# Kernel tuning notes

Measured on AMD Instinct MI355X. Metric: run time of the kernel, lower is better.

## Reference

```python
import jax, jax.numpy as jnp
import numpy as np

B, S, D, H = 2, 2048, 1024, 16
DK = D // H
NEG_INF = jnp.finfo(jnp.float32).min


def setup_inputs() -> dict:
    key = jax.random.key(0)
    ks = jax.random.split(key, 9)
    mk = lambda k, shp, s=0.02: (jax.random.normal(k, shp, dtype=jnp.float32) * s)
    return {
        "X": jax.random.normal(ks[0], (B, S, D), dtype=jnp.float32),
        "Wq": mk(ks[1], (D, D)), "bq": jnp.zeros((D,), jnp.float32),
        "Wk": mk(ks[2], (D, D)), "bk": jnp.zeros((D,), jnp.float32),
        "Wv": mk(ks[3], (D, D)), "bv": jnp.zeros((D,), jnp.float32),
        "Wo": mk(ks[4], (D, D)), "bo": jnp.zeros((D,), jnp.float32),
        "padding_mask": jnp.zeros((B, S), dtype=jnp.int32),
        "causal_mask": 1,
    }


def reference(X, Wq, bq, Wk, bk, Wv, bv, Wo, bo, padding_mask, causal_mask):
    b, s, d = X.shape
    # QKV projections (torch Linear: x @ W.T + b), split into heads -> [B,H,S,DK]
    proj = lambda W, bias: (X @ W.T + bias).reshape(b, s, H, DK).transpose(0, 2, 1, 3)
    Q, K, V = proj(Wq, bq), proj(Wk, bk), proj(Wv, bv)
    scale = jnp.sqrt(jnp.float32(DK))
    scores = jnp.einsum('bhqd,bhkd->bhqk', Q, K) / scale  # [B,H,S,S]
    if padding_mask is not None:
        scores = jnp.where(padding_mask[:, None, None, :] == 1, NEG_INF, scores)
    if causal_mask:
        causal = jnp.triu(jnp.ones((s, s), dtype=bool), k=1)  # [S,S]
        scores = jnp.where(causal[None, None, :, :], NEG_INF, scores)
    alpha = jax.nn.softmax(scores, axis=-1)  # [B,H,S,S]
    context = jnp.einsum('bhqk,bhkd->bhqd', alpha, V)  # [B,H,S,DK]
    context = context.transpose(0, 2, 1, 3).reshape(b, s, d)
    output = context @ Wo.T + bo
    return output, alpha
```

## Files before the change

kernel.cpp:

```cpp
#include <hip/hip_runtime.h>
#include <cstdint>
#include <cstddef>

#define S_   2048
#define D_   1024
#define H_   16
#define DK_  64
#define BH_  32
#define M_   4096
#define NT_  64
#define NEG_INF_F (-3.4028234663852886e38f)

typedef short bf16x8 __attribute__((ext_vector_type(8)));
typedef float f32x4 __attribute__((ext_vector_type(4)));

__device__ __forceinline__ short f2b(float f) {
  union { float f; uint32_t u; } x; x.f = f;
  uint32_t r = (x.u + 0x7fffu + ((x.u >> 16) & 1u)) >> 16;
  return (short)r;
}

__global__ __launch_bounds__(256) void k_cvt6(
    const float* __restrict__ X,  const float* __restrict__ Wq,
    const float* __restrict__ Wk, const float* __restrict__ Wv,
    const float* __restrict__ Wo, const int* __restrict__ pad,
    short* __restrict__ Xb,  short* __restrict__ Wqb,
    short* __restrict__ Wkb, short* __restrict__ Wvb,
    short* __restrict__ Wob, float* __restrict__ padb) {
  const int job = blockIdx.y;
  const int i = blockIdx.x * 256 + threadIdx.x;
  if (job == 5) {
    if (i < (2 * S_) / 4) {
      int4 p = ((const int4*)pad)[i];
      float4 o;
      o.x = p.x ? NEG_INF_F : 0.f;  o.y = p.y ? NEG_INF_F : 0.f;
      o.z = p.z ? NEG_INF_F : 0.f;  o.w = p.w ? NEG_INF_F : 0.f;
      ((float4*)padb)[i] = o;
    }
    return;
  }
  const float* src = job == 0 ? X : job == 1 ? Wq : job == 2 ? Wk
                   : job == 3 ? Wv : Wo;
  short* dst = job == 0 ? Xb : job == 1 ? Wqb : job == 2 ? Wkb
             : job == 3 ? Wvb : Wob;
  const int n4 = (job == 0) ? (M_ * D_ / 4) : (D_ * D_ / 4);
  if (i < n4) {
    float4 v = ((const float4*)src)[i];
    short4 s;
    s.x = f2b(v.x); s.y = f2b(v.y); s.z = f2b(v.z); s.w = f2b(v.w);
    ((short4*)dst)[i] = s;
  }
}

__global__ __launch_bounds__(256) void k_qkv(
    const short* __restrict__ Ab,
    const short* __restrict__ W0, const short* __restrict__ W1,
    const short* __restrict__ W2,
    const float* __restrict__ b0, const float* __restrict__ b1,
    const float* __restrict__ b2,
    short* __restrict__ o0, short* __restrict__ o1, short* __restrict__ o2) {
  __shared__ short As[128][40];
  __shared__ short Bs[128][40];
  const int z = blockIdx.z;
  const short* Wb = z == 0 ? W0 : z == 1 ? W1 : W2;
  const float* bias = z == 0 ? b0 : z == 1 ? b1 : b2;
  short* outb = z == 0 ? o0 : z == 1 ? o1 : o2;
  const float oscale = (z == 0) ? 0.125f : 1.0f;

  const int flat = blockIdx.x + 8 * blockIdx.y;
  const int xcd = flat & 7, slot = flat >> 3;
  const int m0 = (xcd + 8 * (slot & 3)) * 128;
  const int n0 = (slot >> 2) * 128;

  const int tid = threadIdx.x;
  const int wid = tid >> 6, lane = tid & 63;
  const int lr = lane & 15, lk8 = (lane >> 4) * 8;
  const int wm = (wid >> 1) * 64, wn = (wid & 1) * 64;

  f32x4 acc[4][4] = {};

  for (int kt = 0; kt < D_; kt += 32) {
#pragma unroll
    for (int i = 0; i < 2; ++i) {
      int li = tid + i * 256;
      int r = li >> 2, g = li & 3;
      int4 a = *(const int4*)(Ab + (size_t)(m0 + r) * D_ + kt + g * 8);
      *(int4*)&As[r][g * 8] = a;
      int4 w = *(const int4*)(Wb + (size_t)(n0 + r) * D_ + kt + g * 8);
      *(int4*)&Bs[r][g * 8] = w;
    }
    __syncthreads();

    bf16x8 af[4], bf[4];
#pragma unroll
    for (int x = 0; x < 4; ++x) {
      af[x] = *(const bf16x8*)&As[wm + x * 16 + lr][lk8];
      bf[x] = *(const bf16x8*)&Bs[wn + x * 16 + lr][lk8];
    }
#pragma unroll
    for (int mi = 0; mi < 4; ++mi)
#pragma unroll
      for (int ni = 0; ni < 4; ++ni)
        acc[mi][ni] = __builtin_amdgcn_mfma_f32_16x16x32_bf16(
            af[mi], bf[ni], acc[mi][ni], 0, 0, 0);
    __syncthreads();
  }

#pragma unroll
  for (int mi = 0; mi < 4; ++mi)
#pragma unroll
    for (int ni = 0; ni < 4; ++ni) {
      int n = n0 + wn + ni * 16 + lr;
      float bv = bias[n];
#pragma unroll
      for (int j = 0; j < 4; ++j) {
        int m = m0 + wm + mi * 16 + (lane >> 4) * 4 + j;
        float v = (acc[mi][ni][j] + bv) * oscale;
        int b = m >> 11, s = m & (S_ - 1);
        int h = n >> 6, dk = n & (DK_ - 1);
        outb[(((size_t)(b * H_ + h)) * S_ + s) * DK_ + dk] = f2b(v);
      }
    }
}

__global__ __launch_bounds__(256) void k_vt(const short* __restrict__ V,
                                            short* __restrict__ VT) {
  __shared__ short t[64][72];
  const int tid = threadIdx.x;
  const int bh = blockIdx.y, s0 = blockIdx.x * 64;
  const short* src = V + ((size_t)bh * S_ + s0) * DK_;
#pragma unroll
  for (int i = 0; i < 2; ++i) {
    int li = tid + i * 256;
    int r = li >> 3, g = li & 7;
    int4 v = *(const int4*)(src + r * DK_ + g * 8);
    *(int4*)&t[r][g * 8] = v;
  }
  __syncthreads();
  short* dst = VT + (size_t)bh * DK_ * S_ + s0;
#pragma unroll
  for (int i = 0; i < 2; ++i) {
    int li = tid + i * 256;
    int dkr = li >> 3, g = li & 7;
    short o[8];
#pragma unroll
    for (int j = 0; j < 8; ++j) o[j] = t[g * 8 + j][dkr];
    *(int4*)(dst + (size_t)dkr * S_ + g * 8) = *(int4*)o;
  }
}

__global__ __launch_bounds__(256) void k_apv(const short* __restrict__ Q,
                                             const short* __restrict__ Kb,
                                             const short* __restrict__ VT,
                                             const float* __restrict__ padb,
                                             const int* __restrict__ causalp,
                                             float* __restrict__ alpha,
                                             short* __restrict__ ctxb) {
  __shared__ float red[3][64][32];
  __shared__ float ml[4][32][2];

  const int tid = threadIdx.x, wid = tid >> 6, lane = tid & 63;
  const int id = blockIdx.x;
  const int xcd = id & 7, slot = id >> 3;
  const int bh = 8 * (slot & 3) + xcd;
  const int pair = slot >> 2;
  const int lr = lane & 15, lk8 = (lane >> 4) * 8;
  const int g = lane >> 4, g4 = g * 4;
  const int b = bh >> 4, hh = bh & (H_ - 1);
  const short* Qb = Q + (size_t)bh * S_ * DK_;
  const short* Kp = Kb + (size_t)bh * S_ * DK_;
  const short* VTb = VT + (size_t)bh * DK_ * S_;
  const float* pbias = padb + b * S_;
  float* arow = alpha + (size_t)bh * S_ * S_;

  const int causal = *causalp;

  for (int half = 0; half < 2; ++half) {
    const int tile = half == 0 ? (NT_ - 1 - pair) : pair;
    const int qw = tile * 32;
    const int nsteps = causal ? (tile + 1) : (S_ / 32);

    bf16x8 qf[2][2];
#pragma unroll
    for (int qi = 0; qi < 2; ++qi)
#pragma unroll
      for (int h = 0; h < 2; ++h)
        qf[qi][h] = *(const bf16x8*)(Qb + (size_t)(qw + qi * 16 + lr) * DK_ +
                                     h * 32 + lk8);

    float m[2] = {-1e30f, -1e30f}, l[2] = {0.f, 0.f};

    for (int st = wid; st < nsteps; st += 4) {
      const int kc = st * 32;
      const bool diag = causal && (st == tile);
      float s[2][8];
#pragma unroll
      for (int h2 = 0; h2 < 2; ++h2) {
        const int kcc = kc + h2 * 16;
        bf16x8 kf0 = *(const bf16x8*)(Kp + (size_t)(kcc + lr) * DK_ + lk8);
        bf16x8 kf1 = *(const bf16x8*)(Kp + (size_t)(kcc + lr) * DK_ + 32 + lk8);
        float4 pb = *(const float4*)(pbias + kcc + g4);
#pragma unroll
        for (int qi = 0; qi < 2; ++qi) {
          f32x4 z = {0.f, 0.f, 0.f, 0.f};
          z = __builtin_amdgcn_mfma_f32_16x16x32_bf16(kf0, qf[qi][0], z, 0, 0, 0);
          z = __builtin_amdgcn_mfma_f32_16x16x32_bf16(kf1, qf[qi][1], z, 0, 0, 0);
          const int q = qw + qi * 16 + lr;
#pragma unroll
          for (int j = 0; j < 4; ++j) {
            float sv = z[j] + ((const float*)&pb)[j];
            if (diag && (kcc + g4 + j > q)) sv = NEG_INF_F;
            s[qi][h2 * 4 + j] = sv;
          }
        }
      }
#pragma unroll
      for (int qi = 0; qi < 2; ++qi) {
        float pm = fmaxf(fmaxf(fmaxf(s[qi][0], s[qi][1]), fmaxf(s[qi][2], s[qi][3])),
                         fmaxf(fmaxf(s[qi][4], s[qi][5]), fmaxf(s[qi][6], s[qi][7])));
        const float mn = fmaxf(m[qi], pm);
        float sum = 0.f;
#pragma unroll
        for (int jj = 0; jj < 8; ++jj) sum += __expf(s[qi][jj] - mn);
        l[qi] = l[qi] * __expf(m[qi] - mn) + sum;
        m[qi] = mn;
      }
    }

#pragma unroll
    for (int off = 16; off <= 32; off <<= 1) {
#pragma unroll
      for (int qi = 0; qi < 2; ++qi) {
        const float mo = __shfl_xor(m[qi], off);
        const float lo = __shfl_xor(l[qi], off);
        const float mn = fmaxf(m[qi], mo);
        l[qi] = l[qi] * __expf(m[qi] - mn) + lo * __expf(mo - mn);
        m[qi] = mn;
      }
    }
    if (g == 0) {
      ml[wid][lr][0] = m[0];      ml[wid][lr][1] = l[0];
      ml[wid][16 + lr][0] = m[1]; ml[wid][16 + lr][1] = l[1];
    }
    __syncthreads();
    float li[2];
#pragma unroll
    for (int qi = 0; qi < 2; ++qi) {
      const int row = qi * 16 + lr;
      float mf = ml[0][row][0], lf = ml[0][row][1];
#pragma unroll
      for (int w = 1; w < 4; ++w) {
        const float mo = ml[w][row][0], lo = ml[w][row][1];
        const float mn = fmaxf(mf, mo);
        lf = lf * __expf(mf - mn) + lo * __expf(mo - mn);
        mf = mn;
      }
      m[qi] = mf;
      li[qi] = 1.0f / lf;
    }

    f32x4 cacc[2][4] = {};

    for (int st = wid; st < nsteps; st += 4) {
      const int kc = st * 32;
      const bool diag = causal && (st == tile);
      uint32_t pk[2][2][2];
#pragma unroll
      for (int h2 = 0; h2 < 2; ++h2) {
        const int kcc = kc + h2 * 16;
        bf16x8 kf0 = *(const bf16x8*)(Kp + (size_t)(kcc + lr) * DK_ + lk8);
        bf16x8 kf1 = *(const bf16x8*)(Kp + (size_t)(kcc + lr) * DK_ + 32 + lk8);
        float4 pb = *(const float4*)(pbias + kcc + g4);
#pragma unroll
        for (int qi = 0; qi < 2; ++qi) {
          f32x4 z = {0.f, 0.f, 0.f, 0.f};
          z = __builtin_amdgcn_mfma_f32_16x16x32_bf16(kf0, qf[qi][0], z, 0, 0, 0);
          z = __builtin_amdgcn_mfma_f32_16x16x32_bf16(kf1, qf[qi][1], z, 0, 0, 0);
          const int q = qw + qi * 16 + lr;
          float a[4];
#pragma unroll
          for (int j = 0; j < 4; ++j) {
            float sv = z[j] + ((const float*)&pb)[j];
            if (diag && (kcc + g4 + j > q)) sv = NEG_INF_F;
            a[j] = __expf(sv - m[qi]) * li[qi];
          }
          *(float4*)(arow + (size_t)q * S_ + kcc + g4) =
              make_float4(a[0], a[1], a[2], a[3]);
          asm volatile("v_cvt_pk_bf16_f32 %0, %1, %2"
                       : "=v"(pk[qi][h2][0]) : "v"(a[0]), "v"(a[1]));
          asm volatile("v_cvt_pk_bf16_f32 %0, %1, %2"
                       : "=v"(pk[qi][h2][1]) : "v"(a[2]), "v"(a[3]));
        }
      }

      bf16x8 paf[2];
#pragma unroll
      for (int qi = 0; qi < 2; ++qi) {
        const uint32_t x00 = pk[qi][0][0], x01 = pk[qi][0][1];
        const uint32_t x10 = pk[qi][1][0], x11 = pk[qi][1][1];
        const uint32_t y00 = __shfl_xor((int)x00, 32);
        const uint32_t y01 = __shfl_xor((int)x01, 32);
        const uint32_t y10 = __shfl_xor((int)x10, 32);
        const uint32_t y11 = __shfl_xor((int)x11, 32);
        const bool hi2 = (g >= 2);
        const uint32_t a0 = hi2 ? x10 : x00, a1 = hi2 ? x11 : x01;
        const uint32_t b0 = hi2 ? y10 : y00, b1 = hi2 ? y11 : y01;
        const uint32_t cA0 = __shfl_xor((int)a0, 16);
        const uint32_t cA1 = __shfl_xor((int)a1, 16);
        const uint32_t cB0 = __shfl_xor((int)b0, 16);
        const uint32_t cB1 = __shfl_xor((int)b1, 16);
        const bool sel_a = (g == 0) || (g == 3);
        const uint32_t u0 = sel_a ? a0 : b0, u1 = sel_a ? a1 : b1;
        const uint32_t v0 = sel_a ? cA0 : cB0, v1 = sel_a ? cA1 : cB1;
        const bool odd = g & 1;
        union { uint32_t u[4]; bf16x8 v; } uu;
        uu.u[0] = odd ? v0 : u0;  uu.u[1] = odd ? v1 : u1;
        uu.u[2] = odd ? u0 : v0;  uu.u[3] = odd ? u1 : v1;
        paf[qi] = uu.v;
      }

#pragma unroll
      for (int di = 0; di < 4; ++di) {
        bf16x8 vf = *(const bf16x8*)(VTb + (size_t)(di * 16 + lr) * S_ + kc + lk8);
        cacc[0][di] = __builtin_amdgcn_mfma_f32_16x16x32_bf16(paf[0], vf,
                                                              cacc[0][di], 0, 0, 0);
        cacc[1][di] = __builtin_amdgcn_mfma_f32_16x16x32_bf16(paf[1], vf,
                                                              cacc[1][di], 0, 0, 0);
      }
    }

    if (causal) {
      const int kz = qw + 32;
      const int c4 = (S_ - kz) >> 2;
#pragma unroll
      for (int rr = 0; rr < 8; ++rr) {
        const int r = wid * 8 + rr;
        float4* bp = (float4*)(arow + (size_t)(qw + r) * S_ + kz);
        for (int i = lane; i < c4; i += 64) bp[i] = make_float4(0.f, 0.f, 0.f, 0.f);
      }
    }

    __syncthreads();
    if (wid > 0) {
#pragma unroll
      for (int qi = 0; qi < 2; ++qi)
#pragma unroll
        for (int di = 0; di < 4; ++di)
#pragma unroll
          for (int j = 0; j < 4; ++j)
            red[wid - 1][lane][qi * 16 + di * 4 + j] = cacc[qi][di][j];
    }
    __syncthreads();
    if (wid == 0) {
#pragma unroll
      for (int w = 0; w < 3; ++w)
#pragma unroll
        for (int qi = 0; qi < 2; ++qi)
#pragma unroll
          for (int di = 0; di < 4; ++di)
#pragma unroll
            for (int j = 0; j < 4; ++j)
              cacc[qi][di][j] += red[w][lane][qi * 16 + di * 4 + j];

#pragma unroll
      for (int qi = 0; qi < 2; ++qi)
#pragma unroll
        for (int di = 0; di < 4; ++di)
#pragma unroll
          for (int j = 0; j < 4; ++j) {
            const int q = qw + qi * 16 + g4 + j;
            const int dk = di * 16 + lr;
            ctxb[((size_t)(b * S_ + q)) * D_ + hh * DK_ + dk] =
                f2b(cacc[qi][di][j]);
          }
    }
    __syncthreads();
  }
}

__global__ __launch_bounds__(256) void k_oproj(const short* __restrict__ Ab,
                                               const short* __restrict__ Wb,
                                               const float* __restrict__ bias,
                                               float* __restrict__ outf) {
  __shared__ short As[128][40];
  __shared__ short Bs[128][40];
  const int flat = blockIdx.x + 8 * blockIdx.y;
  const int xcd = flat & 7, slot = flat >> 3;
  const int m0 = (xcd + 8 * (slot & 3)) * 128;
  const int n0 = (slot >> 2) * 128;

  const int tid = threadIdx.x;
  const int wid = tid >> 6, lane = tid & 63;
  const int lr = lane & 15, lk8 = (lane >> 4) * 8;
  const int wm = (wid >> 1) * 64, wn = (wid & 1) * 64;

  f32x4 acc[4][4] = {};

  for (int kt = 0; kt < D_; kt += 32) {
#pragma unroll
    for (int i = 0; i < 2; ++i) {
      int li = tid + i * 256;
      int r = li >> 2, g = li & 3;
      int4 a = *(const int4*)(Ab + (size_t)(m0 + r) * D_ + kt + g * 8);
      *(int4*)&As[r][g * 8] = a;
      int4 w = *(const int4*)(Wb + (size_t)(n0 + r) * D_ + kt + g * 8);
      *(int4*)&Bs[r][g * 8] = w;
    }
    __syncthreads();

    bf16x8 af[4], bf[4];
#pragma unroll
    for (int x = 0; x < 4; ++x) {
      af[x] = *(const bf16x8*)&As[wm + x * 16 + lr][lk8];
      bf[x] = *(const bf16x8*)&Bs[wn + x * 16 + lr][lk8];
    }
#pragma unroll
    for (int mi = 0; mi < 4; ++mi)
#pragma unroll
      for (int ni = 0; ni < 4; ++ni)
        acc[mi][ni] = __builtin_amdgcn_mfma_f32_16x16x32_bf16(
            af[mi], bf[ni], acc[mi][ni], 0, 0, 0);
    __syncthreads();
  }

#pragma unroll
  for (int mi = 0; mi < 4; ++mi)
#pragma unroll
    for (int ni = 0; ni < 4; ++ni) {
      int n = n0 + wn + ni * 16 + lr;
      float bv = bias[n];
#pragma unroll
      for (int j = 0; j < 4; ++j) {
        int mm = m0 + wm + mi * 16 + (lane >> 4) * 4 + j;
        outf[(size_t)mm * D_ + n] = acc[mi][ni][j] + bv;
      }
    }
}

extern "C" void kernel_launch(void* const* d_in, const int* in_sizes, int n_in,
                              void* d_out, int out_size, void* d_ws,
                              size_t ws_size, hipStream_t stream) {
  (void)in_sizes; (void)n_in; (void)out_size; (void)ws_size;
  const float* X  = (const float*)d_in[0];
  const float* Wq = (const float*)d_in[1];
  const float* bq = (const float*)d_in[2];
  const float* Wk = (const float*)d_in[3];
  const float* bk = (const float*)d_in[4];
  const float* Wv = (const float*)d_in[5];
  const float* bv = (const float*)d_in[6];
  const float* Wo = (const float*)d_in[7];
  const float* bo = (const float*)d_in[8];
  const int* pad    = (const int*)d_in[9];
  const int* causal = (const int*)d_in[10];

  float* out   = (float*)d_out;
  float* alpha = out + (size_t)2 * S_ * D_;

  short* wsb = (short*)d_ws;
  const size_t MM = (size_t)1 << 20;
  short* Xb   = wsb;
  short* Wqb  = wsb + 4 * MM;
  short* Wkb  = wsb + 5 * MM;
  short* Wvb  = wsb + 6 * MM;
  short* Wob  = wsb + 7 * MM;
  short* Qb   = wsb + 8 * MM;
  short* Kb   = wsb + 12 * MM;
  short* Vb   = wsb + 16 * MM;
  short* VTb  = wsb + 20 * MM;
  short* ctxb = wsb + 24 * MM;
  float* padb = (float*)(wsb + 28 * MM);

  dim3 blk(256);

  k_cvt6<<<dim3(4096, 6), blk, 0, stream>>>(X, Wq, Wk, Wv, Wo, pad,
                                            Xb, Wqb, Wkb, Wvb, Wob, padb);

  k_qkv<<<dim3(D_ / 128, M_ / 128, 3), blk, 0, stream>>>(
      Xb, Wqb, Wkb, Wvb, bq, bk, bv, Qb, Kb, Vb);

  k_vt<<<dim3(S_ / 64, BH_), blk, 0, stream>>>(Vb, VTb);

  k_apv<<<dim3(NT_ * BH_ / 2), blk, 0, stream>>>(Qb, Kb, VTb, padb, causal,
                                                 alpha, ctxb);

  k_oproj<<<dim3(D_ / 128, M_ / 128), blk, 0, stream>>>(ctxb, Wob, bo, out);
}
```

Measured before the change: 319.5 us.

## Fuse V transpose into QKV epilogue, use exp2 softmax, widen key step

```diff
diff --git a/kernel.cpp b/kernel.cpp
--- a/kernel.cpp
+++ b/kernel.cpp
@@ -10,6 +10,7 @@
 #define M_   4096
 #define NT_  64
 #define NEG_INF_F (-3.4028234663852886e38f)
+#define QSCALE_F 0.1803368801111137f
 
 typedef short bf16x8 __attribute__((ext_vector_type(8)));
 typedef float f32x4 __attribute__((ext_vector_type(4)));
@@ -64,8 +65,7 @@
   const int z = blockIdx.z;
   const short* Wb = z == 0 ? W0 : z == 1 ? W1 : W2;
   const float* bias = z == 0 ? b0 : z == 1 ? b1 : b2;
-  short* outb = z == 0 ? o0 : z == 1 ? o1 : o2;
-  const float oscale = (z == 0) ? 0.125f : 1.0f;
+  const float oscale = (z == 0) ? QSCALE_F : 1.0f;
 
   const int flat = blockIdx.x + 8 * blockIdx.y;
   const int xcd = flat & 7, slot = flat >> 3;
@@ -75,6 +75,7 @@
   const int tid = threadIdx.x;
   const int wid = tid >> 6, lane = tid & 63;
   const int lr = lane & 15, lk8 = (lane >> 4) * 8;
+  const int g4 = (lane >> 4) * 4;
   const int wm = (wid >> 1) * 64, wn = (wid & 1) * 64;
 
   f32x4 acc[4][4] = {};
@@ -83,11 +84,11 @@
 #pragma unroll
     for (int i = 0; i < 2; ++i) {
       int li = tid + i * 256;
-      int r = li >> 2, g = li & 3;
-      int4 a = *(const int4*)(Ab + (size_t)(m0 + r) * D_ + kt + g * 8);
-      *(int4*)&As[r][g * 8] = a;
-      int4 w = *(const int4*)(Wb + (size_t)(n0 + r) * D_ + kt + g * 8);
-      *(int4*)&Bs[r][g * 8] = w;
+      int r = li >> 2, gg = li & 3;
+      int4 a = *(const int4*)(Ab + (size_t)(m0 + r) * D_ + kt + gg * 8);
+      *(int4*)&As[r][gg * 8] = a;
+      int4 w = *(const int4*)(Wb + (size_t)(n0 + r) * D_ + kt + gg * 8);
+      *(int4*)&Bs[r][gg * 8] = w;
     }
     __syncthreads();
 
@@ -112,41 +113,28 @@
     for (int ni = 0; ni < 4; ++ni) {
       int n = n0 + wn + ni * 16 + lr;
       float bv = bias[n];
-#pragma unroll
-      for (int j = 0; j < 4; ++j) {
-        int m = m0 + wm + mi * 16 + (lane >> 4) * 4 + j;
-        float v = (acc[mi][ni][j] + bv) * oscale;
-        int b = m >> 11, s = m & (S_ - 1);
+      if (z == 2) {
+        int mbase = m0 + wm + mi * 16 + g4;
+        int bb = mbase >> 11, s = mbase & (S_ - 1);
         int h = n >> 6, dk = n & (DK_ - 1);
-        outb[(((size_t)(b * H_ + h)) * S_ + s) * DK_ + dk] = f2b(v);
-      }
-    }
-}
-
-__global__ __launch_bounds__(256) void k_vt(const short* __restrict__ V,
-                                            short* __restrict__ VT) {
-  __shared__ short t[64][72];
-  const int tid = threadIdx.x;
-  const int bh = blockIdx.y, s0 = blockIdx.x * 64;
-  const short* src = V + ((size_t)bh * S_ + s0) * DK_;
-#pragma unroll
-  for (int i = 0; i < 2; ++i) {
-    int li = tid + i * 256;
-    int r = li >> 3, g = li & 7;
-    int4 v = *(const int4*)(src + r * DK_ + g * 8);
-    *(int4*)&t[r][g * 8] = v;
-  }
-  __syncthreads();
-  short* dst = VT + (size_t)bh * DK_ * S_ + s0;
-#pragma unroll
-  for (int i = 0; i < 2; ++i) {
-    int li = tid + i * 256;
-    int dkr = li >> 3, g = li & 7;
-    short o[8];
-#pragma unroll
-    for (int j = 0; j < 8; ++j) o[j] = t[g * 8 + j][dkr];
-    *(int4*)(dst + (size_t)dkr * S_ + g * 8) = *(int4*)o;
-  }
+        short4 o;
+        o.x = f2b(acc[mi][ni][0] + bv);
+        o.y = f2b(acc[mi][ni][1] + bv);
+        o.z = f2b(acc[mi][ni][2] + bv);
+        o.w = f2b(acc[mi][ni][3] + bv);
+        *(short4*)(o2 + (((size_t)(bb * H_ + h)) * DK_ + dk) * S_ + s) = o;
+      } else {
+        short* outb = (z == 0) ? o0 : o1;
+#pragma unroll
+        for (int j = 0; j < 4; ++j) {
+          int m = m0 + wm + mi * 16 + g4 + j;
+          float v = (acc[mi][ni][j] + bv) * oscale;
+          int bb = m >> 11, s = m & (S_ - 1);
+          int h = n >> 6, dk = n & (DK_ - 1);
+          outb[(((size_t)(bb * H_ + h)) * S_ + s) * DK_ + dk] = f2b(v);
+        }
+      }
+    }
 }
 
 __global__ __launch_bounds__(256) void k_apv(const short* __restrict__ Q,
@@ -179,6 +167,7 @@
     const int tile = half == 0 ? (NT_ - 1 - pair) : pair;
     const int qw = tile * 32;
     const int nsteps = causal ? (tile + 1) : (S_ / 32);
+    const int N = (nsteps + 1) >> 1;
 
     bf16x8 qf[2][2];
 #pragma unroll
@@ -190,12 +179,12 @@
 
     float m[2] = {-1e30f, -1e30f}, l[2] = {0.f, 0.f};
 
-    for (int st = wid; st < nsteps; st += 4) {
-      const int kc = st * 32;
-      const bool diag = causal && (st == tile);
-      float s[2][8];
-#pragma unroll
-      for (int h2 = 0; h2 < 2; ++h2) {
+    for (int st = wid; st < N; st += 4) {
+      const int kc = st * 64;
+      const bool diag = causal && (2 * st + 1 >= tile);
+      float s[2][16];
+#pragma unroll
+      for (int h2 = 0; h2 < 4; ++h2) {
         const int kcc = kc + h2 * 16;
         bf16x8 kf0 = *(const bf16x8*)(Kp + (size_t)(kcc + lr) * DK_ + lk8);
         bf16x8 kf1 = *(const bf16x8*)(Kp + (size_t)(kcc + lr) * DK_ + 32 + lk8);
@@ -216,13 +205,16 @@
       }
 #pragma unroll
       for (int qi = 0; qi < 2; ++qi) {
-        float pm = fmaxf(fmaxf(fmaxf(s[qi][0], s[qi][1]), fmaxf(s[qi][2], s[qi][3])),
-                         fmaxf(fmaxf(s[qi][4], s[qi][5]), fmaxf(s[qi][6], s[qi][7])));
+        float p0 = fmaxf(fmaxf(s[qi][0], s[qi][1]), fmaxf(s[qi][2], s[qi][3]));
+        float p1 = fmaxf(fmaxf(s[qi][4], s[qi][5]), fmaxf(s[qi][6], s[qi][7]));
+        float p2 = fmaxf(fmaxf(s[qi][8], s[qi][9]), fmaxf(s[qi][10], s[qi][11]));
+        float p3 = fmaxf(fmaxf(s[qi][12], s[qi][13]), fmaxf(s[qi][14], s[qi][15]));
+        const float pm = fmaxf(fmaxf(p0, p1), fmaxf(p2, p3));
         const float mn = fmaxf(m[qi], pm);
         float sum = 0.f;
 #pragma unroll
-        for (int jj = 0; jj < 8; ++jj) sum += __expf(s[qi][jj] - mn);
-        l[qi] = l[qi] * __expf(m[qi] - mn) + sum;
+        for (int jj = 0; jj < 16; ++jj) sum += exp2f(s[qi][jj] - mn);
+        l[qi] = l[qi] * exp2f(m[qi] - mn) + sum;
         m[qi] = mn;
       }
     }
@@ -234,7 +226,7 @@
         const float mo = __shfl_xor(m[qi], off);
         const float lo = __shfl_xor(l[qi], off);
         const float mn = fmaxf(m[qi], mo);
-        l[qi] = l[qi] * __expf(m[qi] - mn) + lo * __expf(mo - mn);
+        l[qi] = l[qi] * exp2f(m[qi] - mn) + lo * exp2f(mo - mn);
         m[qi] = mn;
       }
     }
@@ -252,7 +244,7 @@
       for (int w = 1; w < 4; ++w) {
         const float mo = ml[w][row][0], lo = ml[w][row][1];
         const float mn = fmaxf(mf, mo);
-        lf = lf * __expf(mf - mn) + lo * __expf(mo - mn);
+        lf = lf * exp2f(mf - mn) + lo * exp2f(mo - mn);
         mf = mn;
       }
       m[qi] = mf;
@@ -261,12 +253,12 @@
 
     f32x4 cacc[2][4] = {};
 
-    for (int st = wid; st < nsteps; st += 4) {
-      const int kc = st * 32;
-      const bool diag = causal && (st == tile);
-      uint32_t pk[2][2][2];
-#pragma unroll
-      for (int h2 = 0; h2 < 2; ++h2) {
+    for (int st = wid; st < N; st += 4) {
+      const int kc = st * 64;
+      const bool diag = causal && (2 * st + 1 >= tile);
+      uint32_t pk[2][4][2];
+#pragma unroll
+      for (int h2 = 0; h2 < 4; ++h2) {
         const int kcc = kc + h2 * 16;
         bf16x8 kf0 = *(const bf16x8*)(Kp + (size_t)(kcc + lr) * DK_ + lk8);
         bf16x8 kf1 = *(const bf16x8*)(Kp + (size_t)(kcc + lr) * DK_ + 32 + lk8);
@@ -282,7 +274,7 @@
           for (int j = 0; j < 4; ++j) {
             float sv = z[j] + ((const float*)&pb)[j];
             if (diag && (kcc + g4 + j > q)) sv = NEG_INF_F;
-            a[j] = __expf(sv - m[qi]) * li[qi];
+            a[j] = exp2f(sv - m[qi]) * li[qi];
           }
           *(float4*)(arow + (size_t)q * S_ + kcc + g4) =
               make_float4(a[0], a[1], a[2], a[3]);
@@ -293,39 +285,43 @@
         }
       }
 
-      bf16x8 paf[2];
-#pragma unroll
-      for (int qi = 0; qi < 2; ++qi) {
-        const uint32_t x00 = pk[qi][0][0], x01 = pk[qi][0][1];
-        const uint32_t x10 = pk[qi][1][0], x11 = pk[qi][1][1];
-        const uint32_t y00 = __shfl_xor((int)x00, 32);
-        const uint32_t y01 = __shfl_xor((int)x01, 32);
-        const uint32_t y10 = __shfl_xor((int)x10, 32);
-        const uint32_t y11 = __shfl_xor((int)x11, 32);
-        const bool hi2 = (g >= 2);
-        const uint32_t a0 = hi2 ? x10 : x00, a1 = hi2 ? x11 : x01;
-        const uint32_t b0 = hi2 ? y10 : y00, b1 = hi2 ? y11 : y01;
-        const uint32_t cA0 = __shfl_xor((int)a0, 16);
-        const uint32_t cA1 = __shfl_xor((int)a1, 16);
-        const uint32_t cB0 = __shfl_xor((int)b0, 16);
-        const uint32_t cB1 = __shfl_xor((int)b1, 16);
-        const bool sel_a = (g == 0) || (g == 3);
-        const uint32_t u0 = sel_a ? a0 : b0, u1 = sel_a ? a1 : b1;
-        const uint32_t v0 = sel_a ? cA0 : cB0, v1 = sel_a ? cA1 : cB1;
-        const bool odd = g & 1;
-        union { uint32_t u[4]; bf16x8 v; } uu;
-        uu.u[0] = odd ? v0 : u0;  uu.u[1] = odd ? v1 : u1;
-        uu.u[2] = odd ? u0 : v0;  uu.u[3] = odd ? u1 : v1;
-        paf[qi] = uu.v;
-      }
-
-#pragma unroll
-      for (int di = 0; di < 4; ++di) {
-        bf16x8 vf = *(const bf16x8*)(VTb + (size_t)(di * 16 + lr) * S_ + kc + lk8);
-        cacc[0][di] = __builtin_amdgcn_mfma_f32_16x16x32_bf16(paf[0], vf,
-                                                              cacc[0][di], 0, 0, 0);
-        cacc[1][di] = __builtin_amdgcn_mfma_f32_16x16x32_bf16(paf[1], vf,
-                                                              cacc[1][di], 0, 0, 0);
+#pragma unroll
+      for (int c = 0; c < 2; ++c) {
+        bf16x8 paf[2];
+#pragma unroll
+        for (int qi = 0; qi < 2; ++qi) {
+          const uint32_t x00 = pk[qi][2 * c][0], x01 = pk[qi][2 * c][1];
+          const uint32_t x10 = pk[qi][2 * c + 1][0], x11 = pk[qi][2 * c + 1][1];
+          const uint32_t y00 = __shfl_xor((int)x00, 32);
+          const uint32_t y01 = __shfl_xor((int)x01, 32);
+          const uint32_t y10 = __shfl_xor((int)x10, 32);
+          const uint32_t y11 = __shfl_xor((int)x11, 32);
+          const bool hi2 = (g >= 2);
+          const uint32_t a0 = hi2 ? x10 : x00, a1 = hi2 ? x11 : x01;
+          const uint32_t b0 = hi2 ? y10 : y00, b1 = hi2 ? y11 : y01;
+          const uint32_t cA0 = __shfl_xor((int)a0, 16);
+          const uint32_t cA1 = __shfl_xor((int)a1, 16);
+          const uint32_t cB0 = __shfl_xor((int)b0, 16);
+          const uint32_t cB1 = __shfl_xor((int)b1, 16);
+          const bool sel_a = (g == 0) || (g == 3);
+          const uint32_t u0 = sel_a ? a0 : b0, u1 = sel_a ? a1 : b1;
+          const uint32_t v0 = sel_a ? cA0 : cB0, v1 = sel_a ? cA1 : cB1;
+          const bool odd = g & 1;
+          union { uint32_t u[4]; bf16x8 v; } uu;
+          uu.u[0] = odd ? v0 : u0;  uu.u[1] = odd ? v1 : u1;
+          uu.u[2] = odd ? u0 : v0;  uu.u[3] = odd ? u1 : v1;
+          paf[qi] = uu.v;
+        }
+        const int kcc2 = kc + c * 32;
+#pragma unroll
+        for (int di = 0; di < 4; ++di) {
+          bf16x8 vf =
+              *(const bf16x8*)(VTb + (size_t)(di * 16 + lr) * S_ + kcc2 + lk8);
+          cacc[0][di] = __builtin_amdgcn_mfma_f32_16x16x32_bf16(
+              paf[0], vf, cacc[0][di], 0, 0, 0);
+          cacc[1][di] = __builtin_amdgcn_mfma_f32_16x16x32_bf16(
+              paf[1], vf, cacc[1][di], 0, 0, 0);
+        }
       }
     }
 
@@ -400,11 +396,11 @@
 #pragma unroll
     for (int i = 0; i < 2; ++i) {
       int li = tid + i * 256;
-      int r = li >> 2, g = li & 3;
-      int4 a = *(const int4*)(Ab + (size_t)(m0 + r) * D_ + kt + g * 8);
-      *(int4*)&As[r][g * 8] = a;
-      int4 w = *(const int4*)(Wb + (size_t)(n0 + r) * D_ + kt + g * 8);
-      *(int4*)&Bs[r][g * 8] = w;
+      int r = li >> 2, gg = li & 3;
+      int4 a = *(const int4*)(Ab + (size_t)(m0 + r) * D_ + kt + gg * 8);
+      *(int4*)&As[r][gg * 8] = a;
+      int4 w = *(const int4*)(Wb + (size_t)(n0 + r) * D_ + kt + gg * 8);
+      *(int4*)&Bs[r][gg * 8] = w;
     }
     __syncthreads();
 
@@ -465,10 +461,9 @@
   short* Wob  = wsb + 7 * MM;
   short* Qb   = wsb + 8 * MM;
   short* Kb   = wsb + 12 * MM;
-  short* Vb   = wsb + 16 * MM;
-  short* VTb  = wsb + 20 * MM;
-  short* ctxb = wsb + 24 * MM;
-  float* padb = (float*)(wsb + 28 * MM);
+  short* VTb  = wsb + 16 * MM;
+  short* ctxb = wsb + 20 * MM;
+  float* padb = (float*)(wsb + 24 * MM);
 
   dim3 blk(256);
 
@@ -476,9 +471,7 @@
                                             Xb, Wqb, Wkb, Wvb, Wob, padb);
 
   k_qkv<<<dim3(D_ / 128, M_ / 128, 3), blk, 0, stream>>>(
-      Xb, Wqb, Wkb, Wvb, bq, bk, bv, Qb, Kb, Vb);
-
-  k_vt<<<dim3(S_ / 64, BH_), blk, 0, stream>>>(Vb, VTb);
+      Xb, Wqb, Wkb, Wvb, bq, bk, bv, Qb, Kb, VTb);
 
   k_apv<<<dim3(NT_ * BH_ / 2), blk, 0, stream>>>(Qb, Kb, VTb, padb, causal,
                                                  alpha, ctxb);
```

Measured after the change: 287.7 us. 1.11x faster.
